# Optimization experiments

Hardware: AMD Instinct MI355X
Metric: run time of the kernel (lower is better)

The kernel has to match this reference:

```python
import jax, jax.numpy as jnp
import numpy as np

INPUT_DIM = 1024
OUTPUT_DIM = 1024
NUM_HEADS = 16  # NOTE: torch .split(num_heads) => chunk SIZE = num_heads
N_CHUNKS = OUTPUT_DIM // NUM_HEADS  # 64 effective heads of dim 16
NEG_INF = -1e9


def setup_inputs() -> dict:
    key = jax.random.key(0)
    k1, k2, k3, k4 = jax.random.split(key, 4)
    B, S = 32, 256
    x = jax.random.normal(k1, (B, S, INPUT_DIM), dtype=jnp.float32)
    mask = jnp.ones((B, S), dtype=jnp.float32)
    # xavier-uniform-ish linear weights, torch layout [out, in]
    lim = float(np.sqrt(6.0 / (INPUT_DIM + OUTPUT_DIM)))
    Wq = jax.random.uniform(k2, (OUTPUT_DIM, INPUT_DIM), jnp.float32, -lim, lim)
    Wk = jax.random.uniform(k3, (OUTPUT_DIM, INPUT_DIM), jnp.float32, -lim, lim)
    Wv = jax.random.uniform(k4, (OUTPUT_DIM, INPUT_DIM), jnp.float32, -lim, lim)
    return {"batch_sequence": x, "sequence_mask": mask, "Wq": Wq, "Wk": Wk, "Wv": Wv}


def _split_heads(m):
    # [B,S,D] -> chunks of size NUM_HEADS stacked in dim 0: [C,B,S,H]
    B, S, D = m.shape
    return jnp.transpose(m.reshape(B, S, N_CHUNKS, NUM_HEADS), (2, 0, 1, 3))


def reference(batch_sequence, sequence_mask, Wq, Wk, Wv):
    q = _split_heads(batch_sequence @ Wq.T)  # [C,B,S,H]
    k = _split_heads(batch_sequence @ Wk.T)
    v = _split_heads(batch_sequence @ Wv.T)
    logits = jnp.einsum("cbqh,cbkh->cbqk", q, k) / jnp.sqrt(
        jnp.asarray(OUTPUT_DIM, batch_sequence.dtype)
    )
    mask2d = sequence_mask[:, :, None] * sequence_mask[:, None, :]  # [B,S,S]
    logits = jnp.where(mask2d[None] > 0, logits, NEG_INF)
    w = jax.nn.softmax(logits, axis=-1)
    out = jnp.einsum("cbqk,cbkh->cbqh", w, v)  # [C,B,S,H]
    B, S = batch_sequence.shape[:2]
    return jnp.transpose(out, (1, 2, 0, 3)).reshape(B, S, OUTPUT_DIM)
```

## Files before the change

kernel.cpp:

```cpp
#include <hip/hip_runtime.h>


typedef unsigned short u16;
typedef unsigned int u32;
typedef __attribute__((ext_vector_type(8))) short short8;
typedef __attribute__((ext_vector_type(4))) short short4v;
typedef __attribute__((ext_vector_type(4))) float floatx4;

#if __has_builtin(__builtin_amdgcn_mfma_f32_16x16x16bf16_1k)
#define MFMA16(A, B, C) __builtin_amdgcn_mfma_f32_16x16x16bf16_1k(A, B, C, 0, 0, 0)
#elif __has_builtin(__builtin_amdgcn_mfma_f32_16x16x16_bf16)
#define MFMA16(A, B, C) __builtin_amdgcn_mfma_f32_16x16x16_bf16(A, B, C, 0, 0, 0)
#else
__device__ __forceinline__ floatx4 mfma16_asm(short4v a, short4v b, floatx4 c) {
  floatx4 d;
  asm volatile("v_mfma_f32_16x16x16_bf16 %0, %1, %2, %3"
               : "=v"(d) : "v"(a), "v"(b), "v"(c));
  return d;
}
#define MFMA16(A, B, C) mfma16_asm(A, B, C)
#endif

#if __has_builtin(__builtin_amdgcn_exp2f)
#define EXP2(x) __builtin_amdgcn_exp2f(x)
#else
#define EXP2(x) __expf((x) * 0.6931471805599453f)
#endif

#define QSCALE 0.045084220f

__device__ __forceinline__ u16 f2bf(float f) {
  union { float f; u32 u; } x; x.f = f;
  u32 r = x.u + 0x7fffu + ((x.u >> 16) & 1u);
  return (u16)(r >> 16);
}
__device__ __forceinline__ float bf2f(u16 u) {
  union { u32 u; float f; } x; x.u = ((u32)u) << 16;
  return x.f;
}

__device__ __forceinline__ void gload16(const void* g, void* l) {
  typedef __attribute__((address_space(1))) const unsigned int gq;
  typedef __attribute__((address_space(3))) unsigned int lq;
  __builtin_amdgcn_global_load_lds((gq*)(size_t)g, (lq*)(size_t)l, 16, 0, 0);
}

#define GM 8192
#define GN 3072
#define GK 1024
#define CSTR 136
#define QKVSEG (64 * 32 * 4096)

__global__ __launch_bounds__(256) void cast_all(const float* __restrict__ x,
                                                const float* __restrict__ wq,
                                                const float* __restrict__ wk,
                                                const float* __restrict__ wv,
                                                u16* __restrict__ XB,
                                                u16* __restrict__ WB) {
  int bid = blockIdx.x;
  const float* src; u16* dst; int off;
  if (bid < 8192)       { src = x;  dst = XB;                 off = bid; }
  else if (bid < 9216)  { src = wq; dst = WB;                 off = bid - 8192; }
  else if (bid < 10240) { src = wk; dst = WB + 1024 * 1024;   off = bid - 9216; }
  else                  { src = wv; dst = WB + 2 * 1024 * 1024; off = bid - 10240; }
  int i = (off * 256 + threadIdx.x) * 4;
  float4 v = *(const float4*)(src + i);
  u32 lo = (u32)f2bf(v.x) | ((u32)f2bf(v.y) << 16);
  u32 hi = (u32)f2bf(v.z) | ((u32)f2bf(v.w) << 16);
  uint2 o; o.x = lo; o.y = hi;
  *(uint2*)(dst + i) = o;
}

__global__ __launch_bounds__(256) void gemm_qkv(const u16* __restrict__ A,
                                                const u16* __restrict__ B,
                                                u16* __restrict__ QKV) {
  __shared__ u16 smem[17408];
  u16* As = smem;
  u16* Bs = smem + 128 * 64;

  const int t = threadIdx.x;
  const int lid = blockIdx.x;
  const int xcd = lid & 7;
  const int slot = lid >> 3;
  const int m0 = (xcd * 8 + (slot & 7)) * 128;
  const int n0 = (slot >> 3) * 128;

  const int wave = t >> 6;
  const int lane = t & 63;
  const int wm = (wave >> 1) * 64;
  const int wn = (wave & 1) * 64;
  const int lrow = lane & 15;
  const int quad = lane >> 4;

  const int r_loc = lane >> 3;
  const int xb = (lane & 7) ^ r_loc;

  floatx4 acc[4][4] = {};

  const size_t arow = (size_t)(m0 + wave * 32 + r_loc) * GK + xb * 8;
  const size_t brow = (size_t)(n0 + wave * 32 + r_loc) * GK + xb * 8;

  for (int k0 = 0; k0 < GK; k0 += 64) {
    __syncthreads();
#pragma unroll
    for (int i = 0; i < 4; i++) {
      gload16(A + arow + (size_t)i * 8 * GK + k0, As + (wave * 32 + i * 8) * 64);
      gload16(B + brow + (size_t)i * 8 * GK + k0, Bs + (wave * 32 + i * 8) * 64);
    }
    __syncthreads();
#pragma unroll
    for (int kk = 0; kk < 2; kk++) {
      short8 af[4], bf[4];
#pragma unroll
      for (int i = 0; i < 4; i++) {
        int row = wm + i * 16 + lrow;
        int pos = ((kk * 4 + quad) ^ (lane & 7)) * 8;
        af[i] = *(const short8*)(As + row * 64 + pos);
      }
#pragma unroll
      for (int j = 0; j < 4; j++) {
        int row = wn + j * 16 + lrow;
        int pos = ((kk * 4 + quad) ^ (lane & 7)) * 8;
        bf[j] = *(const short8*)(Bs + row * 64 + pos);
      }
#pragma unroll
      for (int i = 0; i < 4; i++)
#pragma unroll
        for (int j = 0; j < 4; j++)
          acc[i][j] = __builtin_amdgcn_mfma_f32_16x16x32_bf16(af[i], bf[j], acc[i][j], 0, 0, 0);
    }
  }

  __syncthreads();
  u16* Cs = smem;

  const float qsc = (n0 < 1024) ? QSCALE : 1.0f;

  const int crow0 = quad * 4;
  const int ccol = lane & 15;
#pragma unroll
  for (int i = 0; i < 4; i++)
#pragma unroll
    for (int j = 0; j < 4; j++)
#pragma unroll
      for (int r = 0; r < 4; r++)
        Cs[(wm + i * 16 + crow0 + r) * CSTR + wn + j * 16 + ccol] = f2bf(acc[i][j][r] * qsc);
  __syncthreads();

  const int qkv = n0 >> 10;
  const int c0 = (n0 >> 4) & 63;
  const int b = m0 >> 8;
  const int s0 = m0 & 255;
  const int s = t >> 1;
  const int hh = (t & 1) * 8;

#pragma unroll
  for (int g = 0; g < 8; g++) {
    uint4 val = *(const uint4*)(Cs + s * CSTR + g * 16 + hh);
    size_t base = (((size_t)(qkv * 64 + c0 + g) * 32 + b) * 256 + (s0 + s)) * 16 + hh;
    *(uint4*)(QKV + base) = val;
  }
}

template <bool MASKED>
__device__ __forceinline__ void attn_loop(const u16* __restrict__ Kp,
                                          const u16* __restrict__ Vp,
                                          const short4v* bq, const float* mqv,
                                          const float* m_s,
                                          floatx4* oacc, floatx4* lacc,
                                          int col, int quad) {
  const short4v ones = {(short)0x3F80, (short)0x3F80, (short)0x3F80, (short)0x3F80};
#pragma unroll 2
  for (int kt = 0; kt < 16; kt++) {
    const int kb = kt * 16;
    short4v ak = *(const short4v*)(Kp + (kb + col) * 16 + quad * 4);
    short4v av;
#pragma unroll
    for (int i = 0; i < 4; i++)
      av[i] = (short)Vp[(kb + quad * 4 + i) * 16 + col];
    float mk[4];
    if (MASKED) {
#pragma unroll
      for (int i = 0; i < 4; i++) mk[i] = m_s[kb + quad * 4 + i];
    }
#pragma unroll
    for (int qt = 0; qt < 4; qt++) {
      floatx4 z = {0.f, 0.f, 0.f, 0.f};
      floatx4 st = MFMA16(ak, bq[qt], z);
      float e[4];
#pragma unroll
      for (int i = 0; i < 4; i++) {
        e[i] = EXP2(st[i]);
        if (MASKED) e[i] = (mqv[qt] * mk[i] > 0.f) ? e[i] : 0.f;
      }
      union { u32 u[2]; short4v s; } pk;
      pk.u[0] = __builtin_amdgcn_perm(__float_as_uint(e[1]), __float_as_uint(e[0]), 0x07060302u);
      pk.u[1] = __builtin_amdgcn_perm(__float_as_uint(e[3]), __float_as_uint(e[2]), 0x07060302u);
      lacc[qt] = MFMA16(ones, pk.s, lacc[qt]);
      oacc[qt] = MFMA16(av, pk.s, oacc[qt]);
    }
  }
}

__global__ __launch_bounds__(256) void attn_kernel(const u16* __restrict__ QKV,
                                                   const float* __restrict__ mask,
                                                   float* __restrict__ out) {
  __shared__ float m_s[256];
  __shared__ float l_s[256];
  __shared__ float ot[16 * 257];

  const int c = blockIdx.x;
  const int b = blockIdx.y;
  const int t = threadIdx.x;
  const int wave = t >> 6;
  const int lane = t & 63;
  const int col = lane & 15;
  const int quad = lane >> 4;

  const size_t hb = ((size_t)c * 32 + b) * 4096;
  const u16* Qp = QKV + hb;
  const u16* Kp = QKV + QKVSEG + hb;
  const u16* Vp = QKV + 2 * QKVSEG + hb;

  float mv = mask[b * 256 + t];
  m_s[t] = mv;
  const int allones = __syncthreads_and(mv > 0.f);

  const int q0 = wave * 64;

  short4v bq[4];
#pragma unroll
  for (int qt = 0; qt < 4; qt++)
    bq[qt] = *(const short4v*)(Qp + (q0 + qt * 16 + col) * 16 + quad * 4);

  float mqv[4];
#pragma unroll
  for (int qt = 0; qt < 4; qt++) mqv[qt] = m_s[q0 + qt * 16 + col];

  floatx4 oacc[4] = {};
  floatx4 lacc[4] = {};

  if (allones)
    attn_loop<false>(Kp, Vp, bq, mqv, m_s, oacc, lacc, col, quad);
  else
    attn_loop<true>(Kp, Vp, bq, mqv, m_s, oacc, lacc, col, quad);

#pragma unroll
  for (int qt = 0; qt < 4; qt++) {
    if (quad == 0) l_s[q0 + qt * 16 + col] = lacc[qt][0];
#pragma unroll
    for (int r = 0; r < 4; r++)
      ot[(quad * 4 + r) * 257 + q0 + qt * 16 + col] = oacc[qt][r];
  }
  __syncthreads();

  float l = l_s[t];
  float* op = out + ((size_t)b * 256 + t) * 1024 + c * 16;
  float o[16];
  if (allones || l > 0.f) {
    float inv = 1.0f / l;
#pragma unroll
    for (int h = 0; h < 16; h++) o[h] = ot[h * 257 + t] * inv;
  } else {
#pragma unroll
    for (int h = 0; h < 16; h++) o[h] = 0.f;
    for (int k = 0; k < 256; k++)
#pragma unroll
      for (int h = 0; h < 16; h++) o[h] += bf2f(Vp[k * 16 + h]);
#pragma unroll
    for (int h = 0; h < 16; h++) o[h] *= (1.0f / 256.0f);
  }
#pragma unroll
  for (int g = 0; g < 4; g++) {
    float4 r;
    r.x = o[g * 4 + 0]; r.y = o[g * 4 + 1]; r.z = o[g * 4 + 2]; r.w = o[g * 4 + 3];
    *(float4*)(op + g * 4) = r;
  }
}

extern "C" void kernel_launch(void* const* d_in, const int* in_sizes, int n_in,
                              void* d_out, int out_size, void* d_ws, size_t ws_size,
                              hipStream_t stream) {
  const float* x    = (const float*)d_in[0];
  const float* mask = (const float*)d_in[1];
  const float* Wq   = (const float*)d_in[2];
  const float* Wk   = (const float*)d_in[3];
  const float* Wv   = (const float*)d_in[4];
  float* out = (float*)d_out;

  u16* XB  = (u16*)d_ws;
  u16* WB  = XB + (size_t)GM * GK;
  u16* QKV = WB + (size_t)GN * GK;

  cast_all<<<11264, 256, 0, stream>>>(x, Wq, Wk, Wv, XB, WB);
  gemm_qkv<<<1536, 256, 0, stream>>>(XB, WB, QKV);
  attn_kernel<<<dim3(64, 32), 256, 0, stream>>>(QKV, mask, out);
}
```

Baseline: 187.5 us.

## Fuse QKV projection GEMM into per-head attention kernel via shared memory

Drops the separate QKV GEMM kernel. Each attention block now computes its own 256x48 Q/K/V slice for one (batch, head) straight from the bf16 inputs and keeps Q, K and a transposed V in LDS. The goal is to cut the global write and re-read of the QKV intermediate and one kernel launch. In exchange, each block re-streams the full batch activation tile, so activation reads grow roughly from 24x to 64x and depend on cache reuse. The narrow 48-wide N tile also has lower MFMA intensity, and one of the four waves sits idle during the weight loads.

```diff
diff --git a/kernel.cpp b/kernel.cpp
--- a/kernel.cpp
+++ b/kernel.cpp
@@ -45,11 +45,9 @@
   __builtin_amdgcn_global_load_lds((gq*)(size_t)g, (lq*)(size_t)l, 16, 0, 0);
 }
 
-#define GM 8192
-#define GN 3072
 #define GK 1024
-#define CSTR 136
-#define QKVSEG (64 * 32 * 4096)
+#define QKS 20
+#define VTS 264
 
 __global__ __launch_bounds__(256) void cast_all(const float* __restrict__ x,
                                                 const float* __restrict__ wq,
@@ -71,113 +69,19 @@
   *(uint2*)(dst + i) = o;
 }
 
-__global__ __launch_bounds__(256) void gemm_qkv(const u16* __restrict__ A,
-                                                const u16* __restrict__ B,
-                                                u16* __restrict__ QKV) {
-  __shared__ u16 smem[17408];
-  u16* As = smem;
-  u16* Bs = smem + 128 * 64;
-
-  const int t = threadIdx.x;
-  const int lid = blockIdx.x;
-  const int xcd = lid & 7;
-  const int slot = lid >> 3;
-  const int m0 = (xcd * 8 + (slot & 7)) * 128;
-  const int n0 = (slot >> 3) * 128;
-
-  const int wave = t >> 6;
-  const int lane = t & 63;
-  const int wm = (wave >> 1) * 64;
-  const int wn = (wave & 1) * 64;
-  const int lrow = lane & 15;
-  const int quad = lane >> 4;
-
-  const int r_loc = lane >> 3;
-  const int xb = (lane & 7) ^ r_loc;
-
-  floatx4 acc[4][4] = {};
-
-  const size_t arow = (size_t)(m0 + wave * 32 + r_loc) * GK + xb * 8;
-  const size_t brow = (size_t)(n0 + wave * 32 + r_loc) * GK + xb * 8;
-
-  for (int k0 = 0; k0 < GK; k0 += 64) {
-    __syncthreads();
-#pragma unroll
-    for (int i = 0; i < 4; i++) {
-      gload16(A + arow + (size_t)i * 8 * GK + k0, As + (wave * 32 + i * 8) * 64);
-      gload16(B + brow + (size_t)i * 8 * GK + k0, Bs + (wave * 32 + i * 8) * 64);
-    }
-    __syncthreads();
-#pragma unroll
-    for (int kk = 0; kk < 2; kk++) {
-      short8 af[4], bf[4];
-#pragma unroll
-      for (int i = 0; i < 4; i++) {
-        int row = wm + i * 16 + lrow;
-        int pos = ((kk * 4 + quad) ^ (lane & 7)) * 8;
-        af[i] = *(const short8*)(As + row * 64 + pos);
-      }
-#pragma unroll
-      for (int j = 0; j < 4; j++) {
-        int row = wn + j * 16 + lrow;
-        int pos = ((kk * 4 + quad) ^ (lane & 7)) * 8;
-        bf[j] = *(const short8*)(Bs + row * 64 + pos);
-      }
-#pragma unroll
-      for (int i = 0; i < 4; i++)
-#pragma unroll
-        for (int j = 0; j < 4; j++)
-          acc[i][j] = __builtin_amdgcn_mfma_f32_16x16x32_bf16(af[i], bf[j], acc[i][j], 0, 0, 0);
-    }
-  }
-
-  __syncthreads();
-  u16* Cs = smem;
-
-  const float qsc = (n0 < 1024) ? QSCALE : 1.0f;
-
-  const int crow0 = quad * 4;
-  const int ccol = lane & 15;
-#pragma unroll
-  for (int i = 0; i < 4; i++)
-#pragma unroll
-    for (int j = 0; j < 4; j++)
-#pragma unroll
-      for (int r = 0; r < 4; r++)
-        Cs[(wm + i * 16 + crow0 + r) * CSTR + wn + j * 16 + ccol] = f2bf(acc[i][j][r] * qsc);
-  __syncthreads();
-
-  const int qkv = n0 >> 10;
-  const int c0 = (n0 >> 4) & 63;
-  const int b = m0 >> 8;
-  const int s0 = m0 & 255;
-  const int s = t >> 1;
-  const int hh = (t & 1) * 8;
-
-#pragma unroll
-  for (int g = 0; g < 8; g++) {
-    uint4 val = *(const uint4*)(Cs + s * CSTR + g * 16 + hh);
-    size_t base = (((size_t)(qkv * 64 + c0 + g) * 32 + b) * 256 + (s0 + s)) * 16 + hh;
-    *(uint4*)(QKV + base) = val;
-  }
-}
-
 template <bool MASKED>
-__device__ __forceinline__ void attn_loop(const u16* __restrict__ Kp,
-                                          const u16* __restrict__ Vp,
+__device__ __forceinline__ void attn_loop(const u16* __restrict__ Ks,
+                                          const u16* __restrict__ Vt,
                                           const short4v* bq, const float* mqv,
                                           const float* m_s,
                                           floatx4* oacc, floatx4* lacc,
                                           int col, int quad) {
   const short4v ones = {(short)0x3F80, (short)0x3F80, (short)0x3F80, (short)0x3F80};
-#pragma unroll 2
+#pragma unroll 4
   for (int kt = 0; kt < 16; kt++) {
     const int kb = kt * 16;
-    short4v ak = *(const short4v*)(Kp + (kb + col) * 16 + quad * 4);
-    short4v av;
-#pragma unroll
-    for (int i = 0; i < 4; i++)
-      av[i] = (short)Vp[(kb + quad * 4 + i) * 16 + col];
+    short4v ak = *(const short4v*)(Ks + (kb + col) * QKS + quad * 4);
+    short4v av = *(const short4v*)(Vt + col * VTS + kb + quad * 4);
     float mk[4];
     if (MASKED) {
 #pragma unroll
@@ -202,36 +106,95 @@
   }
 }
 
-__global__ __launch_bounds__(256) void attn_kernel(const u16* __restrict__ QKV,
-                                                   const float* __restrict__ mask,
-                                                   float* __restrict__ out) {
+__global__ __launch_bounds__(256) void fused_qkv_attn(const u16* __restrict__ XB,
+                                                      const u16* __restrict__ WB,
+                                                      const float* __restrict__ mask,
+                                                      float* __restrict__ out) {
+  __shared__ u16 smem[19456];
   __shared__ float m_s[256];
-  __shared__ float l_s[256];
-  __shared__ float ot[16 * 257];
-
-  const int c = blockIdx.x;
-  const int b = blockIdx.y;
+
+  const int bid = blockIdx.x;
+  const int b = bid & 31;
+  const int c = bid >> 5;
   const int t = threadIdx.x;
   const int wave = t >> 6;
   const int lane = t & 63;
   const int col = lane & 15;
   const int quad = lane >> 4;
 
-  const size_t hb = ((size_t)c * 32 + b) * 4096;
-  const u16* Qp = QKV + hb;
-  const u16* Kp = QKV + QKVSEG + hb;
-  const u16* Vp = QKV + 2 * QKVSEG + hb;
+  u16* Xs = smem;
+  u16* Ws = smem + 16384;
 
   float mv = mask[b * 256 + t];
   m_s[t] = mv;
   const int allones = __syncthreads_and(mv > 0.f);
 
+  const int r_loc = lane >> 3;
+  const int xb = (lane & 7) ^ r_loc;
+
+  floatx4 acc[4][3] = {};
+
+  const size_t xrow = ((size_t)b * 256 + wave * 64 + r_loc) * GK + xb * 8;
+  const int wg0 = wave * 2;
+  int wrow0 = 0, wrow1 = 0;
+  if (wave < 3) {
+    int wr0 = wg0 * 8 + r_loc, wr1 = wr0 + 8;
+    wrow0 = (wr0 >> 4) * 1024 + c * 16 + (wr0 & 15);
+    wrow1 = (wr1 >> 4) * 1024 + c * 16 + (wr1 & 15);
+  }
+
+  for (int k0 = 0; k0 < GK; k0 += 64) {
+    __syncthreads();
+#pragma unroll
+    for (int i = 0; i < 8; i++)
+      gload16(XB + xrow + (size_t)i * 8 * GK + k0, Xs + (wave * 64 + i * 8) * 64);
+    if (wave < 3) {
+      gload16(WB + (size_t)wrow0 * GK + k0 + xb * 8, Ws + (wg0 * 8) * 64);
+      gload16(WB + (size_t)wrow1 * GK + k0 + xb * 8, Ws + (wg0 * 8 + 8) * 64);
+    }
+    __syncthreads();
+#pragma unroll
+    for (int kk = 0; kk < 2; kk++) {
+      const int pos = ((kk * 4 + quad) ^ (lane & 7)) * 8;
+      short8 af[4], bf[3];
+#pragma unroll
+      for (int mt = 0; mt < 4; mt++)
+        af[mt] = *(const short8*)(Xs + (wave * 64 + mt * 16 + col) * 64 + pos);
+#pragma unroll
+      for (int nt = 0; nt < 3; nt++)
+        bf[nt] = *(const short8*)(Ws + (nt * 16 + col) * 64 + pos);
+#pragma unroll
+      for (int mt = 0; mt < 4; mt++)
+#pragma unroll
+        for (int nt = 0; nt < 3; nt++)
+          acc[mt][nt] = __builtin_amdgcn_mfma_f32_16x16x32_bf16(af[mt], bf[nt], acc[mt][nt], 0, 0, 0);
+    }
+  }
+
+  __syncthreads();
+  u16* Qs = smem;
+  u16* Ks = smem + 5120;
+  u16* Vt = smem + 10240;
+  float* l_s = (float*)(smem + 14464);
+
+#pragma unroll
+  for (int mt = 0; mt < 4; mt++) {
+    const int row = wave * 64 + mt * 16 + quad * 4;
+#pragma unroll
+    for (int r = 0; r < 4; r++) {
+      Qs[(row + r) * QKS + col] = f2bf(acc[mt][0][r] * QSCALE);
+      Ks[(row + r) * QKS + col] = f2bf(acc[mt][1][r]);
+      Vt[col * VTS + row + r] = f2bf(acc[mt][2][r]);
+    }
+  }
+  __syncthreads();
+
   const int q0 = wave * 64;
 
   short4v bq[4];
 #pragma unroll
   for (int qt = 0; qt < 4; qt++)
-    bq[qt] = *(const short4v*)(Qp + (q0 + qt * 16 + col) * 16 + quad * 4);
+    bq[qt] = *(const short4v*)(Qs + (q0 + qt * 16 + col) * QKS + quad * 4);
 
   float mqv[4];
 #pragma unroll
@@ -241,9 +204,12 @@
   floatx4 lacc[4] = {};
 
   if (allones)
-    attn_loop<false>(Kp, Vp, bq, mqv, m_s, oacc, lacc, col, quad);
+    attn_loop<false>(Ks, Vt, bq, mqv, m_s, oacc, lacc, col, quad);
   else
-    attn_loop<true>(Kp, Vp, bq, mqv, m_s, oacc, lacc, col, quad);
+    attn_loop<true>(Ks, Vt, bq, mqv, m_s, oacc, lacc, col, quad);
+
+  __syncthreads();
+  float* ot = (float*)smem;
 
 #pragma unroll
   for (int qt = 0; qt < 4; qt++) {
@@ -266,7 +232,7 @@
     for (int h = 0; h < 16; h++) o[h] = 0.f;
     for (int k = 0; k < 256; k++)
 #pragma unroll
-      for (int h = 0; h < 16; h++) o[h] += bf2f(Vp[k * 16 + h]);
+      for (int h = 0; h < 16; h++) o[h] += bf2f(Vt[h * VTS + k]);
 #pragma unroll
     for (int h = 0; h < 16; h++) o[h] *= (1.0f / 256.0f);
   }
@@ -288,11 +254,9 @@
   const float* Wv   = (const float*)d_in[4];
   float* out = (float*)d_out;
 
-  u16* XB  = (u16*)d_ws;
-  u16* WB  = XB + (size_t)GM * GK;
-  u16* QKV = WB + (size_t)GN * GK;
+  u16* XB = (u16*)d_ws;
+  u16* WB = XB + (size_t)8192 * 1024;
 
   cast_all<<<11264, 256, 0, stream>>>(x, Wq, Wk, Wv, XB, WB);
-  gemm_qkv<<<1536, 256, 0, stream>>>(XB, WB, QKV);
-  attn_kernel<<<dim3(64, 32), 256, 0, stream>>>(QKV, mask, out);
-}
+  fused_qkv_attn<<<2048, 256, 0, stream>>>(XB, WB, mask, out);
+}
```

New measurement: 171.7 us. -8.4%, faster.
